# Kernel optimization log

Hardware: AMD Instinct MI355X
Metric: run time of the kernel (lower is better)

The kernel has to match this reference:

```python
import jax, jax.numpy as jnp
import numpy as np

H = 8        # heads
DK = 64      # dim_key
L = 64       # rel_pos_length
BN_EPS = 1e-5


def calc_reindexing_tensor(l, Lr):
    # Appendix B (5): band indicator of shape [l, l, 2L-1]
    x = jnp.arange(l)[:, None, None]
    i = jnp.arange(l)[None, :, None]
    r = jnp.arange(-(Lr - 1), Lr)[None, None, :]
    return ((i - x == r) & (jnp.abs(i - x) <= Lr)).astype(jnp.float32)


def setup_inputs() -> dict:
    key = jax.random.key(0)
    ks = jax.random.split(key, 6)
    b, c, x, y = 8, 256, 64, 64
    dim_hidden = H * DK
    return {
        "img": jax.random.normal(ks[0], (b, c, x, y), jnp.float32),
        "w_qkv": jax.random.normal(ks[1], (dim_hidden * 3, c), jnp.float32) * 0.02,
        "w_out": jax.random.normal(ks[2], (c, dim_hidden), jnp.float32) * 0.02,
        "b_out": jnp.zeros((c,), jnp.float32),
        "rel_rows": jax.random.normal(ks[3], (2 * L - 1, DK), jnp.float32),
        "rel_columns": jax.random.normal(ks[4], (2 * L - 1, DK), jnp.float32),
        "bn_gamma": jnp.ones((DK,), jnp.float32),
        "bn_beta": jnp.zeros((DK,), jnp.float32),
    }


def reference(img, w_qkv, w_out, b_out, rel_rows, rel_columns, bn_gamma, bn_beta):
    b, c, x, y = img.shape
    m = x * y
    # 1x1 conv (no bias) == channel GEMM
    qkv = jnp.einsum('bcxy,oc->boxy', img, w_qkv)
    q, k, v = jnp.split(qkv, 3, axis=1)
    # (b, H*DK, x, y) -> (b*H, DK, x*y)
    q = q.reshape(b * H, DK, m)
    k = k.reshape(b * H, DK, m)
    v = v.reshape(b * H, DK, m)

    # linear-attention content path
    k = jax.nn.softmax(k, axis=-1)
    context = jnp.einsum('ndm,nem->nde', k, v)          # (n, DK, DK)
    content_out = jnp.einsum('nde,ndm->nem', context, q)  # norm_queries=False
    content_out = content_out.reshape(b * H, DK, x, y)

    # relative-position path (dense banded einsums, faithful to original)
    q4 = q.reshape(b * H, DK, x, y)
    v4 = v.reshape(b * H, DK, x, y)
    Ix = calc_reindexing_tensor(x, L)                   # (x, x, 2L-1)
    Px = jnp.einsum('xir,rd->xid', Ix, rel_rows)        # (x, x, DK)
    Sx = jnp.einsum('ndxy,xid->nixy', q4, Px)
    Yh = jnp.einsum('nixy,neiy->nexy', Sx, v4)
    # BatchNorm2d(DK), training-mode batch stats over (n, x, y)
    mean = Yh.mean(axis=(0, 2, 3), keepdims=True)
    var = Yh.var(axis=(0, 2, 3), keepdims=True)
    Yh = (Yh - mean) * jax.lax.rsqrt(var + BN_EPS)
    Yh = Yh * bn_gamma[None, :, None, None] + bn_beta[None, :, None, None]

    Iy = Ix if x == y else calc_reindexing_tensor(y, L)
    Py = jnp.einsum('yir,rd->yid', Iy, rel_columns)     # (y, y, DK)
    Sy = jnp.einsum('ndxy,yid->nixy', q4, Py)
    rel_pos_out = jnp.einsum('nixy,nexi->nexy', Sy, Yh)

    out = content_out + rel_pos_out                     # (b*H, DK, x, y)
    out = out.reshape(b, H * DK, x, y)
    # 1x1 conv with bias
    return jnp.einsum('bcxy,oc->boxy', out, w_out) + b_out[None, :, None, None]
```

## Files before the change

kernel.cpp:

```cpp
#include <hip/hip_runtime.h>
#include <hip/hip_bf16.h>
#include <math.h>

#define NH   64
#define DKC  64
#define MM   4096
#define CC   256
#define RRN  127

typedef __hip_bfloat16 bf16;
__device__ __forceinline__ float b2f(bf16 x) { return __bfloat162float(x); }
__device__ __forceinline__ bf16 f2b(float x) { return __float2bfloat16(x); }
__device__ __forceinline__ unsigned short bbits(float x) { bf16 h = f2b(x); return *(unsigned short*)&h; }
__device__ __forceinline__ float fbits(unsigned short u) { bf16 h = *(bf16*)&u; return b2f(h); }

typedef short bf16x8 __attribute__((ext_vector_type(8)));
typedef float f32x4 __attribute__((ext_vector_type(4)));
typedef unsigned short u16;
typedef u16 u16x4 __attribute__((ext_vector_type(4)));

#define AS1 __attribute__((address_space(1)))
#define AS3 __attribute__((address_space(3)))
#define GLOAD16(gp, lp) __builtin_amdgcn_global_load_lds((const AS1 void*)(gp), (AS3 void*)(lp), 16, 0, 0)

__device__ __forceinline__ int swzsrc(int lane) { return 8 * ((lane & 7) ^ (lane >> 3)); }
#define FRSWZ(kelem, row) ((kelem) ^ (((row) & 7) * 8))

__global__ __launch_bounds__(256) void k_cvt_w(const float* __restrict__ w, bf16* __restrict__ wb) {
  const int i = blockIdx.x * 256 + threadIdx.x;
  wb[i] = f2b(w[i]);
}
__global__ __launch_bounds__(256) void k_cvt_w2(const float* __restrict__ w, bf16* __restrict__ wb) {
  const int i = blockIdx.x * 256 + threadIdx.x;
  wb[i] = f2b(w[i]);
}
__global__ __launch_bounds__(256) void k_cvt_rel(const float* __restrict__ r, bf16* __restrict__ rb) {
  const int i = blockIdx.x * 256 + threadIdx.x;
  rb[i] = (i < RRN * 64) ? f2b(r[i]) : f2b(0.f);
}
__global__ __launch_bounds__(256) void k_cvt_relr(const float* __restrict__ r, bf16* __restrict__ rb) {
  const int i = blockIdx.x * 256 + threadIdx.x;
  if (i < RRN * 64) rb[i] = f2b(r[i]);
}

__global__ __launch_bounds__(256) void k_timg(const float* __restrict__ img, bf16* __restrict__ imgT) {
  const int b = blockIdx.z, c0 = blockIdx.y * 64, m0 = blockIdx.x * 64;
  const int tid = threadIdx.x;
  __shared__ bf16 T[64][65];
  const float* ib = img + ((size_t)b * CC + c0) * MM + m0;
#pragma unroll
  for (int l = 0; l < 16; ++l) {
    int e = tid + l * 256;
    int cc = e >> 6, mm = e & 63;
    T[cc][mm] = f2b(ib[(size_t)cc * MM + mm]);
  }
  __syncthreads();
  bf16* ob = imgT + ((size_t)b * MM + m0) * CC + c0;
#pragma unroll
  for (int l = 0; l < 16; ++l) {
    int e = tid + l * 256;
    int mm = e >> 6, cc = e & 63;
    ob[(size_t)mm * CC + cc] = T[cc][mm];
  }
}

__global__ __launch_bounds__(256) void k_qkv(const bf16* __restrict__ wb, const bf16* __restrict__ imgT,
                                             bf16* __restrict__ q, bf16* __restrict__ kk, bf16* __restrict__ v) {
  const int bI = blockIdx.z;
  const int o0 = blockIdx.y * 128;
  const int m0 = blockIdx.x * 128;
  const int tid = threadIdx.x;
  const int lane = tid & 63, wid = tid >> 6;
  const int fr = lane & 15;
  const int fq = lane >> 4;
  const int wm = (wid >> 1) * 64, wn = (wid & 1) * 64;

  __shared__ __align__(16) short As[128 * 64];
  __shared__ __align__(16) short Bs[128 * 64];

  const bf16* iB = imgT + (size_t)bI * MM * CC;

  f32x4 acc[4][4];
#pragma unroll
  for (int mi = 0; mi < 4; ++mi)
#pragma unroll
    for (int ni = 0; ni < 4; ++ni) acc[mi][ni] = (f32x4){0.f, 0.f, 0.f, 0.f};

  const int srow = lane >> 3;
  const int skc = swzsrc(lane);

  for (int kt = 0; kt < 4; ++kt) {
    const int k0 = kt * 64;
#pragma unroll
    for (int cc = 0; cc < 4; ++cc) {
      const int c = wid * 4 + cc;
      const int r = c * 8 + srow;
      GLOAD16(wb + (size_t)(o0 + r) * CC + k0 + skc, &As[c * 512]);
      GLOAD16(iB + (size_t)(m0 + r) * CC + k0 + skc, &Bs[c * 512]);
    }
    __syncthreads();
    bf16x8 af[4][2], bfr[4][2];
#pragma unroll
    for (int mi = 0; mi < 4; ++mi)
#pragma unroll
      for (int kkk = 0; kkk < 2; ++kkk)
        af[mi][kkk] = *(const bf16x8*)&As[(wm + mi * 16 + fr) * 64 + FRSWZ(kkk * 32 + fq * 8, fr)];
#pragma unroll
    for (int ni = 0; ni < 4; ++ni)
#pragma unroll
      for (int kkk = 0; kkk < 2; ++kkk)
        bfr[ni][kkk] = *(const bf16x8*)&Bs[(wn + ni * 16 + fr) * 64 + FRSWZ(kkk * 32 + fq * 8, fr)];
#pragma unroll
    for (int mi = 0; mi < 4; ++mi)
#pragma unroll
      for (int ni = 0; ni < 4; ++ni)
#pragma unroll
        for (int kkk = 0; kkk < 2; ++kkk)
          acc[mi][ni] = __builtin_amdgcn_mfma_f32_16x16x32_bf16(af[mi][kkk], bfr[ni][kkk], acc[mi][ni], 0, 0, 0);
    __syncthreads();
  }

#pragma unroll
  for (int mi = 0; mi < 4; ++mi) {
#pragma unroll
    for (int ni = 0; ni < 4; ++ni) {
      const int mcol = m0 + wn + ni * 16 + fr;
#pragma unroll
      for (int r = 0; r < 4; ++r) {
        int oo = o0 + wm + mi * 16 + fq * 4 + r;
        bf16* dst;
        if (oo < 512) { dst = q; }
        else if (oo < 1024) { dst = kk; oo -= 512; }
        else { dst = v; oo -= 1024; }
        dst[((size_t)bI * 512 + oo) * MM + mcol] = f2b(acc[mi][ni][r]);
      }
    }
  }
}

__global__ __launch_bounds__(256) void k_softmax(bf16* __restrict__ kk) {
  const size_t row = blockIdx.x;
  bf16* p = kk + row * (size_t)MM;
  const int t = threadIdx.x;
  __shared__ float sred[4];
  float mx = -1e30f;
#pragma unroll
  for (int j = 0; j < 4; ++j) {
    u16x4 v4 = *(const u16x4*)&p[(j * 256 + t) * 4];
#pragma unroll
    for (int k = 0; k < 4; ++k) mx = fmaxf(mx, fbits(v4[k]));
  }
#pragma unroll
  for (int off = 32; off; off >>= 1) mx = fmaxf(mx, __shfl_down(mx, off));
  if ((t & 63) == 0) sred[t >> 6] = mx;
  __syncthreads();
  mx = fmaxf(fmaxf(sred[0], sred[1]), fmaxf(sred[2], sred[3]));
  __syncthreads();
  float s = 0.f;
#pragma unroll
  for (int j = 0; j < 4; ++j) {
    u16x4 v4 = *(const u16x4*)&p[(j * 256 + t) * 4];
    u16x4 o;
#pragma unroll
    for (int k = 0; k < 4; ++k) { float e = expf(fbits(v4[k]) - mx); o[k] = bbits(e); s += e; }
    *(u16x4*)&p[(j * 256 + t) * 4] = o;
  }
#pragma unroll
  for (int off = 32; off; off >>= 1) s += __shfl_down(s, off);
  if ((t & 63) == 0) sred[t >> 6] = s;
  __syncthreads();
  s = sred[0] + sred[1] + sred[2] + sred[3];
  const float inv = 1.0f / s;
#pragma unroll
  for (int j = 0; j < 4; ++j) {
    u16x4 v4 = *(const u16x4*)&p[(j * 256 + t) * 4];
    u16x4 o;
#pragma unroll
    for (int k = 0; k < 4; ++k) o[k] = bbits(fbits(v4[k]) * inv);
    *(u16x4*)&p[(j * 256 + t) * 4] = o;
  }
}

__global__ __launch_bounds__(256) void k_ctx2(const bf16* __restrict__ kk, const bf16* __restrict__ v,
                                              float* __restrict__ part) {
  const int ch = blockIdx.x, n = blockIdx.y;
  const int tid = threadIdx.x;
  const int lane = tid & 63, wid = tid >> 6;
  const int fr = lane & 15, fq = lane >> 4;
  const int wr = (wid >> 1) * 32, wc = (wid & 1) * 32;
  __shared__ __align__(16) short Ks[64 * 64];
  __shared__ __align__(16) short Vs[64 * 64];
  const bf16* kp = kk + (size_t)n * DKC * MM;
  const bf16* vp = v + (size_t)n * DKC * MM;
  const int srow = lane >> 3;
  const int skc = swzsrc(lane);

  f32x4 acc[2][2];
#pragma unroll
  for (int mi = 0; mi < 2; ++mi)
#pragma unroll
    for (int ni = 0; ni < 2; ++ni) acc[mi][ni] = (f32x4){0.f, 0.f, 0.f, 0.f};

  for (int t = 0; t < 16; ++t) {
    const int m0 = ch * 1024 + t * 64;
#pragma unroll
    for (int cc = 0; cc < 4; ++cc) {
      const int c = wid * 4 + cc;
      if (c < 8) {
        const int r = c * 8 + srow;
        GLOAD16(kp + (size_t)r * MM + m0 + skc, &Ks[c * 512]);
      } else {
        const int r = (c - 8) * 8 + srow;
        GLOAD16(vp + (size_t)r * MM + m0 + skc, &Vs[(c - 8) * 512]);
      }
    }
    __syncthreads();
    bf16x8 af[2][2], bf[2][2];
#pragma unroll
    for (int mi = 0; mi < 2; ++mi)
#pragma unroll
      for (int kkx = 0; kkx < 2; ++kkx)
        af[mi][kkx] = *(const bf16x8*)&Ks[(wr + mi * 16 + fr) * 64 + FRSWZ(kkx * 32 + fq * 8, fr)];
#pragma unroll
    for (int ni = 0; ni < 2; ++ni)
#pragma unroll
      for (int kkx = 0; kkx < 2; ++kkx)
        bf[ni][kkx] = *(const bf16x8*)&Vs[(wc + ni * 16 + fr) * 64 + FRSWZ(kkx * 32 + fq * 8, fr)];
#pragma unroll
    for (int mi = 0; mi < 2; ++mi)
#pragma unroll
      for (int ni = 0; ni < 2; ++ni)
#pragma unroll
        for (int kkx = 0; kkx < 2; ++kkx)
          acc[mi][ni] = __builtin_amdgcn_mfma_f32_16x16x32_bf16(af[mi][kkx], bf[ni][kkx], acc[mi][ni], 0, 0, 0);
    __syncthreads();
  }
  float* pb = part + ((size_t)ch * NH + n) * 4096;
#pragma unroll
  for (int mi = 0; mi < 2; ++mi)
#pragma unroll
    for (int ni = 0; ni < 2; ++ni)
#pragma unroll
      for (int r = 0; r < 4; ++r)
        pb[(wr + mi * 16 + fq * 4 + r) * 64 + wc + ni * 16 + fr] = acc[mi][ni][r];
}

__global__ __launch_bounds__(256) void k_ctx_red(const float* __restrict__ part, float* __restrict__ ctx) {
  const int idx = blockIdx.x * 256 + threadIdx.x;
  float s = 0.f;
#pragma unroll
  for (int c = 0; c < 4; ++c) s += part[(size_t)c * 262144 + idx];
  ctx[idx] = s;
}

__global__ __launch_bounds__(256) void k_content2(const float* __restrict__ ctx, const bf16* __restrict__ q,
                                                  bf16* __restrict__ contentT) {
  const int m0 = blockIdx.x * 64, n = blockIdx.y;
  const int bI = n >> 3, h = n & 7;
  const int tid = threadIdx.x;
  const int lane = tid & 63, wid = tid >> 6;
  const int fr = lane & 15, fq = lane >> 4;
  const int wr = (wid >> 1) * 32, wc = (wid & 1) * 32;
  __shared__ __align__(16) bf16 CT[64 * 72];
  __shared__ __align__(16) bf16 Qt[64 * 72];
  const float* cn = ctx + (size_t)n * 4096;
  const bf16* qn = q + (size_t)n * DKC * MM;
#pragma unroll
  for (int l = 0; l < 16; ++l) {
    int idx = tid + l * 256;
    int d = idx >> 6, e = idx & 63;
    CT[e * 72 + (d ^ (8 * (e >> 3)))] = f2b(cn[idx]);
  }
#pragma unroll
  for (int l = 0; l < 16; ++l) {
    int idx = tid + l * 256;
    int d = idx >> 6, mm = idx & 63;
    Qt[mm * 72 + (d ^ (8 * (mm >> 3)))] = qn[(size_t)d * MM + m0 + mm];
  }
  __syncthreads();
  bf16x8 af[2][2], bq[2][2];
#pragma unroll
  for (int mi = 0; mi < 2; ++mi) {
    const int row = wr + mi * 16 + fr;
    const int swz = 8 * (row >> 3);
#pragma unroll
    for (int kk = 0; kk < 2; ++kk)
      af[mi][kk] = *(const bf16x8*)&CT[row * 72 + ((kk * 32 + fq * 8) ^ swz)];
  }
#pragma unroll
  for (int ni = 0; ni < 2; ++ni) {
    const int row = wc + ni * 16 + fr;
    const int swz = 8 * (row >> 3);
#pragma unroll
    for (int kk = 0; kk < 2; ++kk)
      bq[ni][kk] = *(const bf16x8*)&Qt[row * 72 + ((kk * 32 + fq * 8) ^ swz)];
  }
  f32x4 acc[2][2];
#pragma unroll
  for (int mi = 0; mi < 2; ++mi)
#pragma unroll
    for (int ni = 0; ni < 2; ++ni) acc[mi][ni] = (f32x4){0.f, 0.f, 0.f, 0.f};
#pragma unroll
  for (int mi = 0; mi < 2; ++mi)
#pragma unroll
    for (int ni = 0; ni < 2; ++ni)
#pragma unroll
      for (int kk = 0; kk < 2; ++kk)
        acc[mi][ni] = __builtin_amdgcn_mfma_f32_16x16x32_bf16(af[mi][kk], bq[ni][kk], acc[mi][ni], 0, 0, 0);
  bf16* cb = contentT + (size_t)bI * MM * 512;
#pragma unroll
  for (int mi = 0; mi < 2; ++mi)
#pragma unroll
    for (int ni = 0; ni < 2; ++ni) {
      const int mm = wc + ni * 16 + fr;
      u16x4 pk;
#pragma unroll
      for (int r = 0; r < 4; ++r) pk[r] = bbits(acc[mi][ni][r]);
      *(u16x4*)&cb[(size_t)(m0 + mm) * 512 + h * 64 + wr + mi * 16 + fq * 4] = pk;
    }
}

__global__ __launch_bounds__(256) void k_sx2(const bf16* __restrict__ relrb, const bf16* __restrict__ q,
                                             bf16* __restrict__ sxT) {
  const int x = blockIdx.x, n = blockIdx.y;
  const int tid = threadIdx.x;
  const int lane = tid & 63, wid = tid >> 6;
  const int fr = lane & 15, fq = lane >> 4;
  const int wr = (wid >> 1) * 32, wc = (wid & 1) * 32;
  __shared__ __align__(16) bf16 Qt[64 * 72];
  const size_t nb = (size_t)n * DKC * MM;
#pragma unroll
  for (int l = 0; l < 16; ++l) {
    int idx = tid + l * 256;
    int d = idx >> 6, y = idx & 63;
    Qt[y * 72 + (d ^ (8 * (y >> 3)))] = q[nb + (size_t)d * MM + x * 64 + y];
  }
  bf16x8 af[2][2];
#pragma unroll
  for (int mi = 0; mi < 2; ++mi) {
    const int j = wr + mi * 16 + fr + 63 - x;
#pragma unroll
    for (int kk = 0; kk < 2; ++kk)
      af[mi][kk] = *(const bf16x8*)&relrb[(size_t)j * 64 + kk * 32 + fq * 8];
  }
  __syncthreads();
  bf16x8 bq[2][2];
#pragma unroll
  for (int ni = 0; ni < 2; ++ni) {
    const int row = wc + ni * 16 + fr;
    const int swz = 8 * (row >> 3);
#pragma unroll
    for (int kk = 0; kk < 2; ++kk)
      bq[ni][kk] = *(const bf16x8*)&Qt[row * 72 + ((kk * 32 + fq * 8) ^ swz)];
  }
  f32x4 acc[2][2];
#pragma unroll
  for (int mi = 0; mi < 2; ++mi)
#pragma unroll
    for (int ni = 0; ni < 2; ++ni) acc[mi][ni] = (f32x4){0.f, 0.f, 0.f, 0.f};
#pragma unroll
  for (int mi = 0; mi < 2; ++mi)
#pragma unroll
    for (int ni = 0; ni < 2; ++ni)
#pragma unroll
      for (int kk = 0; kk < 2; ++kk)
        acc[mi][ni] = __builtin_amdgcn_mfma_f32_16x16x32_bf16(af[mi][kk], bq[ni][kk], acc[mi][ni], 0, 0, 0);
#pragma unroll
  for (int mi = 0; mi < 2; ++mi)
#pragma unroll
    for (int ni = 0; ni < 2; ++ni) {
      const int yy2 = wc + ni * 16 + fr;
      u16x4 pk;
#pragma unroll
      for (int r = 0; r < 4; ++r) pk[r] = bbits(acc[mi][ni][r]);
      *(u16x4*)&sxT[(((size_t)n * 64 + yy2) * 64 + x) * 64 + wr + mi * 16 + fq * 4] = pk;
    }
}

__global__ __launch_bounds__(256) void k_vt(const bf16* __restrict__ v, bf16* __restrict__ vT) {
  const int eg = blockIdx.x, n = blockIdx.y;
  const int tid = threadIdx.x;
  __shared__ short T[8 * 64 * 66];
  const bf16* vp = v + (size_t)n * DKC * MM + (size_t)eg * 8 * MM;
#pragma unroll
  for (int j = 0; j < 16; ++j) {
    int flat = (j * 256 + tid) * 8;
    int e = flat >> 12, m = flat & 4095;
    int x = m >> 6, y0 = m & 63;
    u16x4 lo = *(const u16x4*)&vp[(size_t)e * MM + m];
    u16x4 hi = *(const u16x4*)&vp[(size_t)e * MM + m + 4];
#pragma unroll
    for (int k = 0; k < 4; ++k) T[(e * 64 + y0 + k) * 66 + x] = (short)lo[k];
#pragma unroll
    for (int k = 0; k < 4; ++k) T[(e * 64 + y0 + 4 + k) * 66 + x] = (short)hi[k];
  }
  __syncthreads();
#pragma unroll
  for (int j = 0; j < 32; ++j) {
    int flat4 = j * 256 + tid;
    int x4 = flat4 & 15, e = (flat4 >> 4) & 7, y = flat4 >> 7;
    u16x4 pk;
#pragma unroll
    for (int r = 0; r < 4; ++r) pk[r] = (u16)T[(e * 64 + y) * 66 + x4 * 4 + r];
    *(u16x4*)&vT[(((size_t)n * 64 + y) * 64 + eg * 8 + e) * 64 + x4 * 4] = pk;
  }
}

__global__ __launch_bounds__(256) void k_yh2(const bf16* __restrict__ vT, const bf16* __restrict__ sxT,
                                             bf16* __restrict__ yhT) {
  const int y = blockIdx.x, n = blockIdx.y;
  const int tid = threadIdx.x;
  const int lane = tid & 63, wid = tid >> 6;
  const int fr = lane & 15, fq = lane >> 4;
  const int wr = (wid >> 1) * 32, wc = (wid & 1) * 32;
  __shared__ __align__(16) short Va[64 * 64];
  __shared__ __align__(16) short Sa[64 * 64];
  const size_t rb = ((size_t)n * 64 + y) * 4096;
  const int srow = lane >> 3;
  const int skc = swzsrc(lane);
#pragma unroll
  for (int cc = 0; cc < 2; ++cc) {
    const int c = wid * 2 + cc;
    const int r = c * 8 + srow;
    GLOAD16(vT + rb + (size_t)r * 64 + skc, &Va[c * 512]);
    GLOAD16(sxT + rb + (size_t)r * 64 + skc, &Sa[c * 512]);
  }
  __syncthreads();
  bf16x8 av[2][2], bs[2][2];
#pragma unroll
  for (int mi = 0; mi < 2; ++mi)
#pragma unroll
    for (int kk = 0; kk < 2; ++kk)
      av[mi][kk] = *(const bf16x8*)&Va[(wr + mi * 16 + fr) * 64 + FRSWZ(kk * 32 + fq * 8, fr)];
#pragma unroll
  for (int ni = 0; ni < 2; ++ni)
#pragma unroll
    for (int kk = 0; kk < 2; ++kk)
      bs[ni][kk] = *(const bf16x8*)&Sa[(wc + ni * 16 + fr) * 64 + FRSWZ(kk * 32 + fq * 8, fr)];
  f32x4 acc[2][2];
#pragma unroll
  for (int mi = 0; mi < 2; ++mi)
#pragma unroll
    for (int ni = 0; ni < 2; ++ni) acc[mi][ni] = (f32x4){0.f, 0.f, 0.f, 0.f};
#pragma unroll
  for (int mi = 0; mi < 2; ++mi)
#pragma unroll
    for (int ni = 0; ni < 2; ++ni)
#pragma unroll
      for (int kk = 0; kk < 2; ++kk)
        acc[mi][ni] = __builtin_amdgcn_mfma_f32_16x16x32_bf16(av[mi][kk], bs[ni][kk], acc[mi][ni], 0, 0, 0);
#pragma unroll
  for (int mi = 0; mi < 2; ++mi)
#pragma unroll
    for (int ni = 0; ni < 2; ++ni) {
      const int xo = wc + ni * 16 + fr;
      u16x4 pk;
#pragma unroll
      for (int r = 0; r < 4; ++r) pk[r] = bbits(acc[mi][ni][r]);
      *(u16x4*)&yhT[rb + (size_t)xo * 64 + wr + mi * 16 + fq * 4] = pk;
    }
}

__global__ __launch_bounds__(256) void k_bnpart2(const bf16* __restrict__ yhT, float* __restrict__ ps,
                                                 float* __restrict__ ps2) {
  const int gg = blockIdx.x, n = blockIdx.y;
  const int t = threadIdx.x;
  const int eq = (t & 15) * 4, rg = t >> 4;
  const bf16* p = yhT + (size_t)n * 262144 + (size_t)gg * 512 * 64;
  float s[4] = {}, s2[4] = {};
  for (int r = rg; r < 512; r += 16) {
    u16x4 v4 = *(const u16x4*)&p[(size_t)r * 64 + eq];
#pragma unroll
    for (int k = 0; k < 4; ++k) { float x = fbits(v4[k]); s[k] += x; s2[k] += x * x; }
  }
  __shared__ float ls[16][64], ls2[16][64];
#pragma unroll
  for (int k = 0; k < 4; ++k) { ls[rg][eq + k] = s[k]; ls2[rg][eq + k] = s2[k]; }
  __syncthreads();
  if (t < 64) {
    float S = 0.f, S2 = 0.f;
#pragma unroll
    for (int g = 0; g < 16; ++g) { S += ls[g][t]; S2 += ls2[g][t]; }
    ps[t * 512 + n * 8 + gg] = S;
    ps2[t * 512 + n * 8 + gg] = S2;
  }
}

__global__ __launch_bounds__(64) void k_bnfin(const float* __restrict__ ps, const float* __restrict__ ps2,
                                              float* __restrict__ mu, float* __restrict__ rs) {
  const int e = threadIdx.x;
  float S = 0.f, S2 = 0.f;
  for (int g = 0; g < 512; ++g) { S += ps[e * 512 + g]; S2 += ps2[e * 512 + g]; }
  const float invN = 1.0f / (NH * (float)MM);
  float m = S * invN;
  float var = S2 * invN - m * m;
  mu[e] = m;
  rs[e] = 1.0f / sqrtf(var + 1e-5f);
}

__global__ __launch_bounds__(256) void k_relcol3(const bf16* __restrict__ q, const bf16* __restrict__ yhT,
                                                 const bf16* __restrict__ relcb, const float* __restrict__ mu,
                                                 const float* __restrict__ rs, const float* __restrict__ gamma,
                                                 const float* __restrict__ beta, bf16* __restrict__ contentT) {
  const int xx = blockIdx.x, n = blockIdx.y;
  const int bI = n >> 3, h = n & 7;
  const int tid = threadIdx.x;
  const int lane = tid & 63, wv = tid >> 6;
  const int fr = lane & 15, fq = lane >> 4;
  __shared__ __align__(16) bf16 smem[4608 + 9216 + 4608];
  bf16* Qt = smem;
  bf16* Scb = smem + 4608;
  bf16* Ysb = smem + 4608 + 9216;
  bf16* DT = smem;

  const size_t nb = (size_t)n * DKC * MM;

#pragma unroll
  for (int l = 0; l < 16; ++l) {
    int idx = tid + l * 256;
    int d = idx >> 6, y = idx & 63;
    Qt[y * 72 + (d ^ (8 * (y >> 3)))] = q[nb + (size_t)d * MM + xx * 64 + y];
  }
#pragma unroll
  for (int l = 0; l < 16; ++l) {
    int idx = tid + l * 256;
    int i = idx >> 6, e = idx & 63;
    float val = (b2f(yhT[nb + (size_t)i * 4096 + xx * 64 + e]) - mu[e]) * rs[e] * gamma[e] + beta[e];
    Ysb[e * 72 + (i ^ (8 * (e >> 3)))] = f2b(val);
  }
  bf16x8 af[2][2];
#pragma unroll
  for (int mi = 0; mi < 2; ++mi)
#pragma unroll
    for (int kk = 0; kk < 2; ++kk)
      af[mi][kk] = *(const bf16x8*)&relcb[(size_t)(wv * 32 + mi * 16 + fr) * 64 + kk * 32 + fq * 8];
  __syncthreads();

  f32x4 acc1[2][4];
#pragma unroll
  for (int mi = 0; mi < 2; ++mi)
#pragma unroll
    for (int ni = 0; ni < 4; ++ni) acc1[mi][ni] = (f32x4){0.f, 0.f, 0.f, 0.f};
  bf16x8 bq[4][2];
#pragma unroll
  for (int ni = 0; ni < 4; ++ni) {
    const int row = ni * 16 + fr;
    const int swz = 8 * (row >> 3);
#pragma unroll
    for (int kk = 0; kk < 2; ++kk)
      bq[ni][kk] = *(const bf16x8*)&Qt[row * 72 + ((kk * 32 + fq * 8) ^ swz)];
  }
#pragma unroll
  for (int mi = 0; mi < 2; ++mi)
#pragma unroll
    for (int ni = 0; ni < 4; ++ni)
#pragma unroll
      for (int kk = 0; kk < 2; ++kk)
        acc1[mi][ni] = __builtin_amdgcn_mfma_f32_16x16x32_bf16(af[mi][kk], bq[ni][kk], acc1[mi][ni], 0, 0, 0);
#pragma unroll
  for (int mi = 0; mi < 2; ++mi)
#pragma unroll
    for (int ni = 0; ni < 4; ++ni)
#pragma unroll
      for (int r = 0; r < 4; ++r)
        Scb[(wv * 32 + mi * 16 + fq * 4 + r) * 72 + ni * 16 + fr] = f2b(acc1[mi][ni][r]);
  __syncthreads();

#pragma unroll
  for (int l = 0; l < 16; ++l) {
    int idx = tid + l * 256;
    int y = idx >> 6, i = idx & 63;
    DT[y * 72 + i] = Scb[(i - y + 63) * 72 + y];
  }
  __syncthreads();

  bf16x8 a2[2], bd[4][2];
  {
    const int row = wv * 16 + fr;
    const int swz = 8 * (row >> 3);
#pragma unroll
    for (int kk = 0; kk < 2; ++kk)
      a2[kk] = *(const bf16x8*)&Ysb[row * 72 + ((kk * 32 + fq * 8) ^ swz)];
  }
#pragma unroll
  for (int ni = 0; ni < 4; ++ni)
#pragma unroll
    for (int kk = 0; kk < 2; ++kk)
      bd[ni][kk] = *(const bf16x8*)&DT[(ni * 16 + fr) * 72 + kk * 32 + fq * 8];
  f32x4 acc2[4];
#pragma unroll
  for (int ni = 0; ni < 4; ++ni) acc2[ni] = (f32x4){0.f, 0.f, 0.f, 0.f};
#pragma unroll
  for (int ni = 0; ni < 4; ++ni)
#pragma unroll
    for (int kk = 0; kk < 2; ++kk)
      acc2[ni] = __builtin_amdgcn_mfma_f32_16x16x32_bf16(a2[kk], bd[ni][kk], acc2[ni], 0, 0, 0);

  bf16* cb = contentT + (size_t)bI * MM * 512;
#pragma unroll
  for (int ni = 0; ni < 4; ++ni) {
    size_t a = (size_t)(xx * 64 + ni * 16 + fr) * 512 + h * 64 + wv * 16 + fq * 4;
    u16x4 pk = *(u16x4*)&cb[a];
#pragma unroll
    for (int r = 0; r < 4; ++r) pk[r] = bbits(fbits(pk[r]) + acc2[ni][r]);
    *(u16x4*)&cb[a] = pk;
  }
}

__global__ __launch_bounds__(256) void k_final(const bf16* __restrict__ wb2, const bf16* __restrict__ cT,
                                               const float* __restrict__ bout, float* __restrict__ dout) {
  const int bI = blockIdx.z;
  const int o0 = blockIdx.y * 128;
  const int m0 = blockIdx.x * 128;
  const int tid = threadIdx.x;
  const int lane = tid & 63, wid = tid >> 6;
  const int fr = lane & 15;
  const int fq = lane >> 4;
  const int wm = (wid >> 1) * 64, wn = (wid & 1) * 64;

  __shared__ __align__(16) short As[128 * 64];
  __shared__ __align__(16) short Bs[128 * 64];

  const bf16* cB = cT + (size_t)bI * MM * 512;

  f32x4 acc[4][4];
#pragma unroll
  for (int mi = 0; mi < 4; ++mi)
#pragma unroll
    for (int ni = 0; ni < 4; ++ni) acc[mi][ni] = (f32x4){0.f, 0.f, 0.f, 0.f};

  const int srow = lane >> 3;
  const int skc = swzsrc(lane);

  for (int kt = 0; kt < 8; ++kt) {
    const int k0 = kt * 64;
#pragma unroll
    for (int cc = 0; cc < 4; ++cc) {
      const int c = wid * 4 + cc;
      const int r = c * 8 + srow;
      GLOAD16(wb2 + (size_t)(o0 + r) * 512 + k0 + skc, &As[c * 512]);
      GLOAD16(cB + (size_t)(m0 + r) * 512 + k0 + skc, &Bs[c * 512]);
    }
    __syncthreads();
    bf16x8 af[4][2], bfr[4][2];
#pragma unroll
    for (int mi = 0; mi < 4; ++mi)
#pragma unroll
      for (int kkk = 0; kkk < 2; ++kkk)
        af[mi][kkk] = *(const bf16x8*)&As[(wm + mi * 16 + fr) * 64 + FRSWZ(kkk * 32 + fq * 8, fr)];
#pragma unroll
    for (int ni = 0; ni < 4; ++ni)
#pragma unroll
      for (int kkk = 0; kkk < 2; ++kkk)
        bfr[ni][kkk] = *(const bf16x8*)&Bs[(wn + ni * 16 + fr) * 64 + FRSWZ(kkk * 32 + fq * 8, fr)];
#pragma unroll
    for (int mi = 0; mi < 4; ++mi)
#pragma unroll
      for (int ni = 0; ni < 4; ++ni)
#pragma unroll
        for (int kkk = 0; kkk < 2; ++kkk)
          acc[mi][ni] = __builtin_amdgcn_mfma_f32_16x16x32_bf16(af[mi][kkk], bfr[ni][kkk], acc[mi][ni], 0, 0, 0);
    __syncthreads();
  }

#pragma unroll
  for (int mi = 0; mi < 4; ++mi) {
#pragma unroll
    for (int ni = 0; ni < 4; ++ni) {
      const int mcol = m0 + wn + ni * 16 + fr;
#pragma unroll
      for (int r = 0; r < 4; ++r) {
        const int oo = o0 + wm + mi * 16 + fq * 4 + r;
        dout[((size_t)bI * 256 + oo) * MM + mcol] = acc[mi][ni][r] + bout[oo];
      }
    }
  }
}

extern "C" void kernel_launch(void* const* d_in, const int* in_sizes, int n_in,
                              void* d_out, int out_size, void* d_ws, size_t ws_size,
                              hipStream_t stream) {
  const float* img = (const float*)d_in[0];
  const float* w_qkv = (const float*)d_in[1];
  const float* w_out = (const float*)d_in[2];
  const float* b_out = (const float*)d_in[3];
  const float* rel_rows = (const float*)d_in[4];
  const float* rel_cols = (const float*)d_in[5];
  const float* gamma = (const float*)d_in[6];
  const float* beta = (const float*)d_in[7];
  float* out = (float*)d_out;

  const size_t SZ = (size_t)NH * DKC * MM;
  bf16* q = (bf16*)d_ws;
  bf16* kbuf = q + SZ;
  bf16* vbuf = kbuf + SZ;
  bf16* imgT = vbuf + SZ;
  float* ctxp = (float*)imgT;
  float* ctx = ctxp + 4 * 262144;
  float* ps = ctx + 262144;
  float* ps2 = ps + 32768;
  float* mu = ps2 + 32768;
  float* rs = mu + 64;
  bf16* wb = imgT + 8388608;
  bf16* sxbuf = wb + 393216;
  bf16* wb2 = sxbuf + SZ;
  bf16* relcb = wb2 + 131072;
  bf16* relrb = relcb + 8192;

  k_cvt_w<<<1536, 256, 0, stream>>>(w_qkv, wb);
  k_cvt_w2<<<512, 256, 0, stream>>>(w_out, wb2);
  k_cvt_rel<<<32, 256, 0, stream>>>(rel_cols, relcb);
  k_cvt_relr<<<32, 256, 0, stream>>>(rel_rows, relrb);
  k_timg<<<dim3(64, 4, 8), 256, 0, stream>>>(img, imgT);
  k_qkv<<<dim3(32, 12, 8), 256, 0, stream>>>(wb, imgT, q, kbuf, vbuf);
  k_softmax<<<4096, 256, 0, stream>>>(kbuf);
  k_ctx2<<<dim3(4, 64), 256, 0, stream>>>(kbuf, vbuf, ctxp);
  k_ctx_red<<<1024, 256, 0, stream>>>(ctxp, ctx);
  k_sx2<<<dim3(64, 64), 256, 0, stream>>>(relrb, q, sxbuf);
  k_vt<<<dim3(8, 64), 256, 0, stream>>>(vbuf, kbuf);
  k_yh2<<<dim3(64, 64), 256, 0, stream>>>(kbuf, sxbuf, vbuf);
  k_bnpart2<<<dim3(8, 64), 256, 0, stream>>>(vbuf, ps, ps2);
  k_bnfin<<<1, 64, 0, stream>>>(ps, ps2, mu, rs);
  k_content2<<<dim3(64, 64), 256, 0, stream>>>(ctx, q, sxbuf);
  k_relcol3<<<dim3(64, 64), 256, 0, stream>>>(q, vbuf, relcb, mu, rs, gamma, beta, sxbuf);
  k_final<<<dim3(32, 2, 8), 256, 0, stream>>>(wb2, sxbuf, b_out, out);
}
```

Measured before the change: 237.7 us.

## Fuse content and relative-column kernels, vectorize transpose, register-cache softmax and weights

Merges the content-path GEMM into the relative-column kernel so the contentT buffer is written once, with no read-modify-write, and one launch plus one q read go away. The image transpose now uses float4 loads and 4-wide packed stores. Softmax keeps its values in registers instead of re-reading global memory twice. The QKV and output GEMMs load weight fragments straight from global memory into registers rather than staging them through LDS, trading LDS traffic for uncoalesced global reads that rely on the cache.

```diff
diff --git a/kernel.cpp b/kernel.cpp
--- a/kernel.cpp
+++ b/kernel.cpp
@@ -46,21 +46,26 @@
 __global__ __launch_bounds__(256) void k_timg(const float* __restrict__ img, bf16* __restrict__ imgT) {
   const int b = blockIdx.z, c0 = blockIdx.y * 64, m0 = blockIdx.x * 64;
   const int tid = threadIdx.x;
-  __shared__ bf16 T[64][65];
+  __shared__ short T[64 * 66];
   const float* ib = img + ((size_t)b * CC + c0) * MM + m0;
 #pragma unroll
-  for (int l = 0; l < 16; ++l) {
-    int e = tid + l * 256;
-    int cc = e >> 6, mm = e & 63;
-    T[cc][mm] = f2b(ib[(size_t)cc * MM + mm]);
+  for (int j = 0; j < 4; ++j) {
+    int f4 = j * 256 + tid;
+    int cc = f4 >> 4, mm4 = (f4 & 15) * 4;
+    f32x4 v = *(const f32x4*)&ib[(size_t)cc * MM + mm4];
+#pragma unroll
+    for (int k = 0; k < 4; ++k) T[cc * 66 + mm4 + k] = (short)bbits(v[k]);
   }
   __syncthreads();
   bf16* ob = imgT + ((size_t)b * MM + m0) * CC + c0;
 #pragma unroll
-  for (int l = 0; l < 16; ++l) {
-    int e = tid + l * 256;
-    int mm = e >> 6, cc = e & 63;
-    ob[(size_t)mm * CC + cc] = T[cc][mm];
+  for (int j = 0; j < 4; ++j) {
+    int f4 = j * 256 + tid;
+    int mm = f4 >> 4, cc4 = (f4 & 15) * 4;
+    u16x4 pk;
+#pragma unroll
+    for (int k = 0; k < 4; ++k) pk[k] = (u16)T[(cc4 + k) * 66 + mm];
+    *(u16x4*)&ob[(size_t)mm * CC + cc4] = pk;
   }
 }
 
@@ -75,7 +80,6 @@
   const int fq = lane >> 4;
   const int wm = (wid >> 1) * 64, wn = (wid & 1) * 64;
 
-  __shared__ __align__(16) short As[128 * 64];
   __shared__ __align__(16) short Bs[128 * 64];
 
   const bf16* iB = imgT + (size_t)bI * MM * CC;
@@ -95,16 +99,16 @@
     for (int cc = 0; cc < 4; ++cc) {
       const int c = wid * 4 + cc;
       const int r = c * 8 + srow;
-      GLOAD16(wb + (size_t)(o0 + r) * CC + k0 + skc, &As[c * 512]);
       GLOAD16(iB + (size_t)(m0 + r) * CC + k0 + skc, &Bs[c * 512]);
     }
+    bf16x8 af[4][2];
+#pragma unroll
+    for (int mi = 0; mi < 4; ++mi)
+#pragma unroll
+      for (int kkk = 0; kkk < 2; ++kkk)
+        af[mi][kkk] = *(const bf16x8*)&wb[(size_t)(o0 + wm + mi * 16 + fr) * CC + k0 + kkk * 32 + fq * 8];
     __syncthreads();
-    bf16x8 af[4][2], bfr[4][2];
-#pragma unroll
-    for (int mi = 0; mi < 4; ++mi)
-#pragma unroll
-      for (int kkk = 0; kkk < 2; ++kkk)
-        af[mi][kkk] = *(const bf16x8*)&As[(wm + mi * 16 + fr) * 64 + FRSWZ(kkk * 32 + fq * 8, fr)];
+    bf16x8 bfr[4][2];
 #pragma unroll
     for (int ni = 0; ni < 4; ++ni)
 #pragma unroll
@@ -143,12 +147,13 @@
   bf16* p = kk + row * (size_t)MM;
   const int t = threadIdx.x;
   __shared__ float sred[4];
+  float v[16];
   float mx = -1e30f;
 #pragma unroll
   for (int j = 0; j < 4; ++j) {
     u16x4 v4 = *(const u16x4*)&p[(j * 256 + t) * 4];
 #pragma unroll
-    for (int k = 0; k < 4; ++k) mx = fmaxf(mx, fbits(v4[k]));
+    for (int k = 0; k < 4; ++k) { v[j * 4 + k] = fbits(v4[k]); mx = fmaxf(mx, v[j * 4 + k]); }
   }
 #pragma unroll
   for (int off = 32; off; off >>= 1) mx = fmaxf(mx, __shfl_down(mx, off));
@@ -158,13 +163,7 @@
   __syncthreads();
   float s = 0.f;
 #pragma unroll
-  for (int j = 0; j < 4; ++j) {
-    u16x4 v4 = *(const u16x4*)&p[(j * 256 + t) * 4];
-    u16x4 o;
-#pragma unroll
-    for (int k = 0; k < 4; ++k) { float e = expf(fbits(v4[k]) - mx); o[k] = bbits(e); s += e; }
-    *(u16x4*)&p[(j * 256 + t) * 4] = o;
-  }
+  for (int i = 0; i < 16; ++i) { v[i] = expf(v[i] - mx); s += v[i]; }
 #pragma unroll
   for (int off = 32; off; off >>= 1) s += __shfl_down(s, off);
   if ((t & 63) == 0) sred[t >> 6] = s;
@@ -173,10 +172,9 @@
   const float inv = 1.0f / s;
 #pragma unroll
   for (int j = 0; j < 4; ++j) {
-    u16x4 v4 = *(const u16x4*)&p[(j * 256 + t) * 4];
     u16x4 o;
 #pragma unroll
-    for (int k = 0; k < 4; ++k) o[k] = bbits(fbits(v4[k]) * inv);
+    for (int k = 0; k < 4; ++k) o[k] = bbits(v[j * 4 + k] * inv);
     *(u16x4*)&p[(j * 256 + t) * 4] = o;
   }
 }
@@ -253,73 +251,6 @@
   ctx[idx] = s;
 }
 
-__global__ __launch_bounds__(256) void k_content2(const float* __restrict__ ctx, const bf16* __restrict__ q,
-                                                  bf16* __restrict__ contentT) {
-  const int m0 = blockIdx.x * 64, n = blockIdx.y;
-  const int bI = n >> 3, h = n & 7;
-  const int tid = threadIdx.x;
-  const int lane = tid & 63, wid = tid >> 6;
-  const int fr = lane & 15, fq = lane >> 4;
-  const int wr = (wid >> 1) * 32, wc = (wid & 1) * 32;
-  __shared__ __align__(16) bf16 CT[64 * 72];
-  __shared__ __align__(16) bf16 Qt[64 * 72];
-  const float* cn = ctx + (size_t)n * 4096;
-  const bf16* qn = q + (size_t)n * DKC * MM;
-#pragma unroll
-  for (int l = 0; l < 16; ++l) {
-    int idx = tid + l * 256;
-    int d = idx >> 6, e = idx & 63;
-    CT[e * 72 + (d ^ (8 * (e >> 3)))] = f2b(cn[idx]);
-  }
-#pragma unroll
-  for (int l = 0; l < 16; ++l) {
-    int idx = tid + l * 256;
-    int d = idx >> 6, mm = idx & 63;
-    Qt[mm * 72 + (d ^ (8 * (mm >> 3)))] = qn[(size_t)d * MM + m0 + mm];
-  }
-  __syncthreads();
-  bf16x8 af[2][2], bq[2][2];
-#pragma unroll
-  for (int mi = 0; mi < 2; ++mi) {
-    const int row = wr + mi * 16 + fr;
-    const int swz = 8 * (row >> 3);
-#pragma unroll
-    for (int kk = 0; kk < 2; ++kk)
-      af[mi][kk] = *(const bf16x8*)&CT[row * 72 + ((kk * 32 + fq * 8) ^ swz)];
-  }
-#pragma unroll
-  for (int ni = 0; ni < 2; ++ni) {
-    const int row = wc + ni * 16 + fr;
-    const int swz = 8 * (row >> 3);
-#pragma unroll
-    for (int kk = 0; kk < 2; ++kk)
-      bq[ni][kk] = *(const bf16x8*)&Qt[row * 72 + ((kk * 32 + fq * 8) ^ swz)];
-  }
-  f32x4 acc[2][2];
-#pragma unroll
-  for (int mi = 0; mi < 2; ++mi)
-#pragma unroll
-    for (int ni = 0; ni < 2; ++ni) acc[mi][ni] = (f32x4){0.f, 0.f, 0.f, 0.f};
-#pragma unroll
-  for (int mi = 0; mi < 2; ++mi)
-#pragma unroll
-    for (int ni = 0; ni < 2; ++ni)
-#pragma unroll
-      for (int kk = 0; kk < 2; ++kk)
-        acc[mi][ni] = __builtin_amdgcn_mfma_f32_16x16x32_bf16(af[mi][kk], bq[ni][kk], acc[mi][ni], 0, 0, 0);
-  bf16* cb = contentT + (size_t)bI * MM * 512;
-#pragma unroll
-  for (int mi = 0; mi < 2; ++mi)
-#pragma unroll
-    for (int ni = 0; ni < 2; ++ni) {
-      const int mm = wc + ni * 16 + fr;
-      u16x4 pk;
-#pragma unroll
-      for (int r = 0; r < 4; ++r) pk[r] = bbits(acc[mi][ni][r]);
-      *(u16x4*)&cb[(size_t)(m0 + mm) * 512 + h * 64 + wr + mi * 16 + fq * 4] = pk;
-    }
-}
-
 __global__ __launch_bounds__(256) void k_sx2(const bf16* __restrict__ relrb, const bf16* __restrict__ q,
                                              bf16* __restrict__ sxT) {
   const int x = blockIdx.x, n = blockIdx.y;
@@ -498,22 +429,25 @@
   rs[e] = 1.0f / sqrtf(var + 1e-5f);
 }
 
-__global__ __launch_bounds__(256) void k_relcol3(const bf16* __restrict__ q, const bf16* __restrict__ yhT,
-                                                 const bf16* __restrict__ relcb, const float* __restrict__ mu,
-                                                 const float* __restrict__ rs, const float* __restrict__ gamma,
-                                                 const float* __restrict__ beta, bf16* __restrict__ contentT) {
+__global__ __launch_bounds__(256) void k_crc(const float* __restrict__ ctx, const bf16* __restrict__ q,
+                                             const bf16* __restrict__ yhT, const bf16* __restrict__ relcb,
+                                             const float* __restrict__ mu, const float* __restrict__ rs,
+                                             const float* __restrict__ gamma, const float* __restrict__ beta,
+                                             bf16* __restrict__ contentT) {
   const int xx = blockIdx.x, n = blockIdx.y;
   const int bI = n >> 3, h = n & 7;
   const int tid = threadIdx.x;
   const int lane = tid & 63, wv = tid >> 6;
   const int fr = lane & 15, fq = lane >> 4;
-  __shared__ __align__(16) bf16 smem[4608 + 9216 + 4608];
+  __shared__ __align__(16) bf16 smem[4608 + 9216 + 4608 + 4608];
   bf16* Qt = smem;
   bf16* Scb = smem + 4608;
   bf16* Ysb = smem + 4608 + 9216;
+  bf16* CT = smem + 4608 + 9216 + 4608;
   bf16* DT = smem;
 
   const size_t nb = (size_t)n * DKC * MM;
+  const float* cn = ctx + (size_t)n * 4096;
 
 #pragma unroll
   for (int l = 0; l < 16; ++l) {
@@ -528,12 +462,18 @@
     float val = (b2f(yhT[nb + (size_t)i * 4096 + xx * 64 + e]) - mu[e]) * rs[e] * gamma[e] + beta[e];
     Ysb[e * 72 + (i ^ (8 * (e >> 3)))] = f2b(val);
   }
-  bf16x8 af[2][2];
-#pragma unroll
-  for (int mi = 0; mi < 2; ++mi)
-#pragma unroll
-    for (int kk = 0; kk < 2; ++kk)
-      af[mi][kk] = *(const bf16x8*)&relcb[(size_t)(wv * 32 + mi * 16 + fr) * 64 + kk * 32 + fq * 8];
+#pragma unroll
+  for (int l = 0; l < 16; ++l) {
+    int idx = tid + l * 256;
+    int d = idx >> 6, e = idx & 63;
+    CT[e * 72 + (d ^ (8 * (e >> 3)))] = f2b(cn[idx]);
+  }
+  bf16x8 afr[2][2];
+#pragma unroll
+  for (int mi = 0; mi < 2; ++mi)
+#pragma unroll
+    for (int kk = 0; kk < 2; ++kk)
+      afr[mi][kk] = *(const bf16x8*)&relcb[(size_t)(wv * 32 + mi * 16 + fr) * 64 + kk * 32 + fq * 8];
   __syncthreads();
 
   f32x4 acc1[2][4];
@@ -556,7 +496,7 @@
     for (int ni = 0; ni < 4; ++ni)
 #pragma unroll
       for (int kk = 0; kk < 2; ++kk)
-        acc1[mi][ni] = __builtin_amdgcn_mfma_f32_16x16x32_bf16(af[mi][kk], bq[ni][kk], acc1[mi][ni], 0, 0, 0);
+        acc1[mi][ni] = __builtin_amdgcn_mfma_f32_16x16x32_bf16(afr[mi][kk], bq[ni][kk], acc1[mi][ni], 0, 0, 0);
 #pragma unroll
   for (int mi = 0; mi < 2; ++mi)
 #pragma unroll
@@ -564,6 +504,14 @@
 #pragma unroll
       for (int r = 0; r < 4; ++r)
         Scb[(wv * 32 + mi * 16 + fq * 4 + r) * 72 + ni * 16 + fr] = f2b(acc1[mi][ni][r]);
+  bf16x8 aCT[2];
+  {
+    const int row = wv * 16 + fr;
+    const int swz = 8 * (row >> 3);
+#pragma unroll
+    for (int kk = 0; kk < 2; ++kk)
+      aCT[kk] = *(const bf16x8*)&CT[row * 72 + ((kk * 32 + fq * 8) ^ swz)];
+  }
   __syncthreads();
 
 #pragma unroll
@@ -574,6 +522,14 @@
   }
   __syncthreads();
 
+  f32x4 acc2[4];
+#pragma unroll
+  for (int ni = 0; ni < 4; ++ni) acc2[ni] = (f32x4){0.f, 0.f, 0.f, 0.f};
+#pragma unroll
+  for (int ni = 0; ni < 4; ++ni)
+#pragma unroll
+    for (int kk = 0; kk < 2; ++kk)
+      acc2[ni] = __builtin_amdgcn_mfma_f32_16x16x32_bf16(aCT[kk], bq[ni][kk], acc2[ni], 0, 0, 0);
   bf16x8 a2[2], bd[4][2];
   {
     const int row = wv * 16 + fr;
@@ -587,9 +543,6 @@
 #pragma unroll
     for (int kk = 0; kk < 2; ++kk)
       bd[ni][kk] = *(const bf16x8*)&DT[(ni * 16 + fr) * 72 + kk * 32 + fq * 8];
-  f32x4 acc2[4];
-#pragma unroll
-  for (int ni = 0; ni < 4; ++ni) acc2[ni] = (f32x4){0.f, 0.f, 0.f, 0.f};
 #pragma unroll
   for (int ni = 0; ni < 4; ++ni)
 #pragma unroll
@@ -600,9 +553,9 @@
 #pragma unroll
   for (int ni = 0; ni < 4; ++ni) {
     size_t a = (size_t)(xx * 64 + ni * 16 + fr) * 512 + h * 64 + wv * 16 + fq * 4;
-    u16x4 pk = *(u16x4*)&cb[a];
-#pragma unroll
-    for (int r = 0; r < 4; ++r) pk[r] = bbits(fbits(pk[r]) + acc2[ni][r]);
+    u16x4 pk;
+#pragma unroll
+    for (int r = 0; r < 4; ++r) pk[r] = bbits(acc2[ni][r]);
     *(u16x4*)&cb[a] = pk;
   }
 }
@@ -618,7 +571,6 @@
   const int fq = lane >> 4;
   const int wm = (wid >> 1) * 64, wn = (wid & 1) * 64;
 
-  __shared__ __align__(16) short As[128 * 64];
   __shared__ __align__(16) short Bs[128 * 64];
 
   const bf16* cB = cT + (size_t)bI * MM * 512;
@@ -638,16 +590,16 @@
     for (int cc = 0; cc < 4; ++cc) {
       const int c = wid * 4 + cc;
       const int r = c * 8 + srow;
-      GLOAD16(wb2 + (size_t)(o0 + r) * 512 + k0 + skc, &As[c * 512]);
       GLOAD16(cB + (size_t)(m0 + r) * 512 + k0 + skc, &Bs[c * 512]);
     }
+    bf16x8 af[4][2];
+#pragma unroll
+    for (int mi = 0; mi < 4; ++mi)
+#pragma unroll
+      for (int kkk = 0; kkk < 2; ++kkk)
+        af[mi][kkk] = *(const bf16x8*)&wb2[(size_t)(o0 + wm + mi * 16 + fr) * 512 + k0 + kkk * 32 + fq * 8];
     __syncthreads();
-    bf16x8 af[4][2], bfr[4][2];
-#pragma unroll
-    for (int mi = 0; mi < 4; ++mi)
-#pragma unroll
-      for (int kkk = 0; kkk < 2; ++kkk)
-        af[mi][kkk] = *(const bf16x8*)&As[(wm + mi * 16 + fr) * 64 + FRSWZ(kkk * 32 + fq * 8, fr)];
+    bf16x8 bfr[4][2];
 #pragma unroll
     for (int ni = 0; ni < 4; ++ni)
 #pragma unroll
@@ -721,7 +673,6 @@
   k_yh2<<<dim3(64, 64), 256, 0, stream>>>(kbuf, sxbuf, vbuf);
   k_bnpart2<<<dim3(8, 64), 256, 0, stream>>>(vbuf, ps, ps2);
   k_bnfin<<<1, 64, 0, stream>>>(ps, ps2, mu, rs);
-  k_content2<<<dim3(64, 64), 256, 0, stream>>>(ctx, q, sxbuf);
-  k_relcol3<<<dim3(64, 64), 256, 0, stream>>>(q, vbuf, relcb, mu, rs, gamma, beta, sxbuf);
+  k_crc<<<dim3(64, 64), 256, 0, stream>>>(ctx, q, vbuf, relcb, mu, rs, gamma, beta, sxbuf);
   k_final<<<dim3(32, 2, 8), 256, 0, stream>>>(wb2, sxbuf, b_out, out);
 }
```

Measured after the change: 262.6 us. +10.5%, slower.
